# Kernel tuning notes

Hardware: AMD Instinct MI355X
Metric: run time of the kernel (lower is better)

## Reference

```python
import jax, jax.numpy as jnp
import numpy as np

EPS = 1e-5
GROUPS = 32


def conv2d(x, w, b):
    # x: [N,C,H,W], w: [O,I,3,3] (or 1x1), stride 1, padding 'same' for 3x3
    kh = w.shape[2]
    pad = (kh - 1) // 2
    y = jax.lax.conv_general_dilated(x, w, (1, 1), ((pad, pad), (pad, pad)),
                                     dimension_numbers=('NCHW', 'OIHW', 'NCHW'))
    return y + b[None, :, None, None]


def group_norm(x, g, b):
    N, C, H, W = x.shape
    xr = x.reshape(N, GROUPS, C // GROUPS, H, W)
    mu = xr.mean(axis=(2, 3, 4), keepdims=True)
    var = xr.var(axis=(2, 3, 4), keepdims=True)
    xr = (xr - mu) / jnp.sqrt(var + EPS)
    return xr.reshape(N, C, H, W) * g[None, :, None, None] + b[None, :, None, None]


def batch_norm(x, g, b):
    # training-mode BatchNorm2d: batch statistics over (N,H,W)
    mu = x.mean(axis=(0, 2, 3), keepdims=True)
    var = x.var(axis=(0, 2, 3), keepdims=True)
    return (x - mu) / jnp.sqrt(var + EPS) * g[None, :, None, None] + b[None, :, None, None]


def binary_activation(x):
    # STE: forward sign(x), backward through piecewise poly out3
    out_fwd = jnp.sign(x)
    m1 = (x < -1).astype(x.dtype)
    m2 = (x < 0).astype(x.dtype)
    m3 = (x < 1).astype(x.dtype)
    out1 = -1.0 * m1 + (x * x + 2.0 * x) * (1.0 - m1)
    out2 = out1 * m2 + (-x * x + 2.0 * x) * (1.0 - m2)
    out3 = out2 * m3 + 1.0 * (1.0 - m3)
    return jax.lax.stop_gradient(out_fwd - out3) + out3


def hard_binary_conv(x, w, b):
    # per-output-channel scaling * sign(w), STE through clipped weights
    scale = jax.lax.stop_gradient(jnp.mean(jnp.abs(w), axis=(1, 2, 3), keepdims=True))
    bw_ng = scale * jnp.sign(w)
    clipped = jnp.clip(w, -1.0, 1.0)
    bw = jax.lax.stop_gradient(bw_ng - clipped) + clipped
    return conv2d(x, bw, b)


def learnable_bias(x, emb, w, b):
    bias = jax.nn.silu(emb) @ w.T + b  # [B, C]
    return x + bias[:, :, None, None]


def _forward(c, x, emb,
             rb_gn1_g, rb_gn1_b, rb_conv1_w, rb_conv1_b, rb_emb_w, rb_emb_b,
             rb_gn2_g, rb_gn2_b, rb_conv2_w, rb_conv2_b,
             m1_w, m1_b, bconv_w, bconv_b, bn_g, bn_b,
             m2_w, m2_b, prelu_a, m3_w, m3_b):
    # ResBlock (skip = Identity since out_channels == channels)
    h = conv2d(jax.nn.silu(group_norm(c, rb_gn1_g, rb_gn1_b)), rb_conv1_w, rb_conv1_b)
    eo = jax.nn.silu(emb) @ rb_emb_w.T + rb_emb_b          # [B, 2*C]
    scale, shift = jnp.split(eo[:, :, None, None], 2, axis=1)
    h = group_norm(h, rb_gn2_g, rb_gn2_b) * (1.0 + scale) + shift
    h = conv2d(jax.nn.silu(h), rb_conv2_w, rb_conv2_b)
    c2 = c + h
    # concat + bias + STE binarize + binary conv + BN + channel-pool residual + PReLU
    xc = jnp.concatenate([x, c2], axis=1)                   # [B, 2C, H, W]
    out = learnable_bias(xc, emb, m1_w, m1_b)
    out = binary_activation(out)
    out = hard_binary_conv(out, bconv_w, bconv_b)
    out = batch_norm(out, bn_g, bn_b)
    N, C2, H, W = xc.shape
    out = out + xc.reshape(N, C2 // 2, 2, H, W).mean(axis=2)  # channel mean pooling
    out = learnable_bias(out, emb, m2_w, m2_b)
    out = jnp.where(out >= 0, out, prelu_a[None, :, None, None] * out)  # PReLU
    out = learnable_bias(out, emb, m3_w, m3_b)
    return out


def setup_inputs() -> dict:
    key = jax.random.key(0)
    ks = jax.random.split(key, 24)
    B, C, EMB, H, W = 8, 128, 512, 64, 64
    IN2 = 2 * C
    n = lambda k, s, sc=0.05: jax.random.normal(k, s, dtype=jnp.float32) * sc
    return {
        'c': jax.random.normal(ks[0], (B, C, H, W), dtype=jnp.float32),
        'x': jax.random.normal(ks[1], (B, C, H, W), dtype=jnp.float32),
        'emb': jax.random.normal(ks[2], (B, EMB), dtype=jnp.float32),
        'rb_gn1_g': jnp.ones((C,), jnp.float32), 'rb_gn1_b': jnp.zeros((C,), jnp.float32),
        'rb_conv1_w': n(ks[3], (C, C, 3, 3)), 'rb_conv1_b': n(ks[4], (C,)),
        'rb_emb_w': n(ks[5], (2 * C, EMB)), 'rb_emb_b': n(ks[6], (2 * C,)),
        'rb_gn2_g': jnp.ones((C,), jnp.float32), 'rb_gn2_b': jnp.zeros((C,), jnp.float32),
        'rb_conv2_w': n(ks[7], (C, C, 3, 3)), 'rb_conv2_b': n(ks[8], (C,)),
        'm1_w': n(ks[9], (IN2, EMB)), 'm1_b': n(ks[10], (IN2,)),
        'bconv_w': jax.random.uniform(ks[11], (C, IN2, 3, 3), dtype=jnp.float32) * 0.001,
        'bconv_b': n(ks[12], (C,)),
        'bn_g': jnp.ones((C,), jnp.float32), 'bn_b': jnp.zeros((C,), jnp.float32),
        'm2_w': n(ks[13], (C, EMB)), 'm2_b': n(ks[14], (C,)),
        'prelu_a': jnp.full((C,), 0.25, jnp.float32),
        'm3_w': n(ks[15], (C, EMB)), 'm3_b': n(ks[16], (C,)),
    }


def reference(c, x, emb,
              rb_gn1_g, rb_gn1_b, rb_conv1_w, rb_conv1_b, rb_emb_w, rb_emb_b,
              rb_gn2_g, rb_gn2_b, rb_conv2_w, rb_conv2_b,
              m1_w, m1_b, bconv_w, bconv_b, bn_g, bn_b,
              m2_w, m2_b, prelu_a, m3_w, m3_b):
    return _forward(c, x, emb,
                    rb_gn1_g, rb_gn1_b, rb_conv1_w, rb_conv1_b, rb_emb_w, rb_emb_b,
                    rb_gn2_g, rb_gn2_b, rb_conv2_w, rb_conv2_b,
                    m1_w, m1_b, bconv_w, bconv_b, bn_g, bn_b,
                    m2_w, m2_b, prelu_a, m3_w, m3_b)
```

## Files before the change

### kernel.cpp

```cpp
#include <hip/hip_runtime.h>
#include <stdint.h>


#define B_   8
#define C_   128
#define C2_  256
#define HW_  4096
#define EMB_ 512
#define EPS_ 1e-5f

typedef int   v16i __attribute__((ext_vector_type(16)));
typedef float v16f __attribute__((ext_vector_type(16)));
typedef short v8s  __attribute__((ext_vector_type(8)));
typedef int   v4i  __attribute__((ext_vector_type(4)));

#define COLB 272
#define ROWB (66 * COLB)
#define LDSZ 55296
#define TSTRIDE 132

__device__ __forceinline__ float silu(float v) {
    return v * __builtin_amdgcn_rcpf(1.f + __expf(-v));
}
__device__ __forceinline__ unsigned short f2bf(float f) {
    unsigned int x = __float_as_uint(f);
    return (unsigned short)((x + 0x7FFFu + ((x >> 16) & 1u)) >> 16);
}
__device__ __forceinline__ int8_t sgn8(float v) {
    return (v > 0.f) ? (int8_t)1 : ((v < 0.f) ? (int8_t)(-1) : (int8_t)0);
}
__device__ __forceinline__ void gld16(char* ldst, const char* gsrc) {
    __builtin_amdgcn_global_load_lds((const unsigned int*)gsrc,
                                     (unsigned int*)ldst, 16, 0, 0);
}

__global__ __launch_bounds__(256) void k_prep(
    const float* __restrict__ w, int8_t* __restrict__ sgn,
    float* __restrict__ alpha, float* __restrict__ bnS, float* __restrict__ bnQ,
    float* __restrict__ gnS, float* __restrict__ gnQ,
    const float* __restrict__ w1, const float* __restrict__ w2,
    unsigned short* __restrict__ Wc1, unsigned short* __restrict__ Wc2,
    const float* __restrict__ emb,
    const float* __restrict__ ew, const float* __restrict__ ebb,
    const float* __restrict__ m1w, const float* __restrict__ m1b,
    const float* __restrict__ m2w, const float* __restrict__ m2b,
    const float* __restrict__ m3w, const float* __restrict__ m3b,
    float* __restrict__ eo, float* __restrict__ b1,
    float* __restrict__ b2, float* __restrict__ b3,
    const float* __restrict__ gin,
    float* __restrict__ g1S, float* __restrict__ g1Q,
    int8_t* __restrict__ S) {
    __shared__ float red[256];
    const int blk = blockIdx.x, tid = threadIdx.x;
    if (blk < 128) {
        const int o = blk;
        if (o == 0 && tid < 128) { bnS[tid] = 0.f; bnQ[tid] = 0.f; }
        if (o == 1) { gnS[tid] = 0.f; }
        if (o == 2) { gnQ[tid] = 0.f; }
        const float* wr = w + (size_t)o * (C2_ * 9);
        float s = 0.f;
        for (int i = tid; i < C2_ * 9; i += 256) s += fabsf(wr[i]);
        red[tid] = s;
        __syncthreads();
        for (int st = 128; st > 0; st >>= 1) {
            if (tid < st) red[tid] += red[tid + st];
            __syncthreads();
        }
        if (tid == 0) alpha[o] = red[0] / (float)(C2_ * 9);
        for (int kk = 0; kk < 9; ++kk) {
            float v = wr[tid * 9 + kk];
            sgn[((size_t)(kk * 16 + (tid >> 4)) * C_ + o) * 16 + (tid & 15)] = sgn8(v);
        }
    } else if (blk < 704) {
        int i = (blk - 128) * 256 + tid;
        int co = i / (C_ * 9);
        int rem = i - co * (C_ * 9);
        int ci = rem / 9, kk = rem - ci * 9;
        size_t d = ((size_t)(kk * 16 + (ci >> 3)) * C_ + co) * 8 + (ci & 7);
        Wc1[d] = f2bf(w1[i]);
        Wc2[d] = f2bf(w2[i]);
    } else if (blk < 896) {
        const int o = (blk - 704) * 4 + (tid >> 6);
        const int l = tid & 63;
        const float* wv;
        float bias;
        float* dst;
        int dstride;
        if (o < 256)      { wv = ew  + (size_t)o * EMB_;              bias = ebb[o];    dst = eo + o;  dstride = 256; }
        else if (o < 512) { int r = o - 256; wv = m1w + (size_t)r * EMB_; bias = m1b[r]; dst = b1 + r; dstride = 256; }
        else if (o < 640) { int r = o - 512; wv = m2w + (size_t)r * EMB_; bias = m2b[r]; dst = b2 + r; dstride = 128; }
        else              { int r = o - 640; wv = m3w + (size_t)r * EMB_; bias = m3b[r]; dst = b3 + r; dstride = 128; }
        const float4 wa = *(const float4*)(wv + 8 * l);
        const float4 wb = *(const float4*)(wv + 8 * l + 4);
#pragma unroll
        for (int b = 0; b < B_; ++b) {
            const float* s = emb + b * EMB_ + 8 * l;
            float4 sa = *(const float4*)(s);
            float4 sb = *(const float4*)(s + 4);
            float p = wa.x * silu(sa.x) + wa.y * silu(sa.y) + wa.z * silu(sa.z) + wa.w * silu(sa.w) +
                      wb.x * silu(sb.x) + wb.y * silu(sb.y) + wb.z * silu(sb.z) + wb.w * silu(sb.w);
#pragma unroll
            for (int off = 32; off > 0; off >>= 1) p += __shfl_down(p, off, 64);
            if (l == 0) dst[b * dstride] = bias + p;
        }
    } else if (blk < 1408) {
        const int idx = blk - 896;
        const int n = idx >> 6, rest = idx & 63, grp = rest >> 1, h = rest & 1;
        const size_t base = ((size_t)(n * C_ + grp * 4)) << 12;
        float sum = 0.f, sq = 0.f;
        const float4* in4 = (const float4*)(gin + base);
        for (int i = tid + h * 2048; i < (h + 1) * 2048; i += 256) {
            float4 v = in4[i];
            sum += v.x + v.y + v.z + v.w;
            sq += v.x * v.x + v.y * v.y + v.z * v.z + v.w * v.w;
        }
#pragma unroll
        for (int off = 32; off > 0; off >>= 1) {
            sum += __shfl_xor(sum, off, 64);
            sq  += __shfl_xor(sq, off, 64);
        }
        if ((tid & 63) == 0) { red[tid >> 6] = sum; red[8 + (tid >> 6)] = sq; }
        __syncthreads();
        if (tid == 0) {
            g1S[h * 256 + n * 32 + grp] = red[0] + red[1] + red[2] + red[3];
            g1Q[h * 256 + n * 32 + grp] = red[8] + red[9] + red[10] + red[11];
        }
    } else {
        const int u = blk - 1408;
        const int n = u >> 1;
        const int row = (u & 1) * 65;
        int4* base = (int4*)(S + (size_t)n * 66 * ROWB + (size_t)row * ROWB);
        const int4 z = make_int4(0, 0, 0, 0);
        for (int i = tid; i < ROWB / 16; i += 256) base[i] = z;
    }
}

__global__ __launch_bounds__(512, 4) void k_conv1(
    const float* __restrict__ cin,
    const unsigned short* __restrict__ Wc,
    const float* __restrict__ bias,
    const float* __restrict__ g1w, const float* __restrict__ g1b,
    const float* __restrict__ g1S, const float* __restrict__ g1Q,
    float* __restrict__ outN,
    float* __restrict__ gnS, float* __restrict__ gnQ) {
    __shared__ __align__(16) char lds[LDSZ];
    __shared__ float chA[128], chB[128];
    const int y = blockIdx.x;
    const int n = blockIdx.y;
    const int tid = threadIdx.x;

    if (tid < 128) {
        const int ch = tid, grp = tid >> 2;
        const float s1 = g1S[n * 32 + grp] + g1S[256 + n * 32 + grp];
        const float q1 = g1Q[n * 32 + grp] + g1Q[256 + n * 32 + grp];
        const float mu = s1 * (1.f / 16384.f);
        const float var = q1 * (1.f / 16384.f) - mu * mu;
        const float rstd = rsqrtf(var + EPS_);
        const float A = g1w[ch] * rstd;
        chA[ch] = A;
        chB[ch] = g1b[ch] - mu * A;
    }
    if (tid < 96) {
        int r = tid / 32, q = tid & 31;
        int c = (q >> 4) ? 65 : 0, o = q & 15;
        *(float4*)(lds + (r * 66 + c) * COLB + o * 16) = make_float4(0.f, 0.f, 0.f, 0.f);
    }
    __syncthreads();

    union F4 { float4 v; float f[4]; };
#pragma unroll
    for (int u = 0; u < 6; ++u) {
        int unit = u * 512 + tid;
        int r = unit >> 10, rem = unit & 1023;
        int cp = rem >> 4, s4 = rem & 15;
        int ch0 = 2 * cp;
        int yy = y - 1 + r;
        char* dst0 = lds + (r * 66 + 4 * s4 + 1) * COLB + 4 * cp;
        if (yy >= 0 && yy < 64) {
            const float* src = cin + (((size_t)(n * C_ + ch0)) << 12) + yy * 64 + 4 * s4;
            F4 fa, fb;
            fa.v = *(const float4*)src;
            fb.v = *(const float4*)(src + HW_);
            const float A0 = chA[ch0], B0 = chB[ch0];
            const float A1 = chA[ch0 + 1], B1 = chB[ch0 + 1];
#pragma unroll
            for (int e = 0; e < 4; ++e) {
                unsigned int lo = f2bf(silu(fa.f[e] * A0 + B0));
                unsigned int hi = f2bf(silu(fb.f[e] * A1 + B1));
                *(unsigned int*)(dst0 + e * COLB) = lo | (hi << 16);
            }
        } else {
#pragma unroll
            for (int e = 0; e < 4; ++e)
                *(unsigned int*)(dst0 + e * COLB) = 0u;
        }
    }
    __syncthreads();

    const int w = tid >> 6;
    const int og = w >> 1;
    const int ph = w & 1;
    const int l = tid & 63;
    const int lm = l & 31;
    const int lh = l >> 5;

    v16f acc;
#pragma unroll
    for (int i = 0; i < 16; ++i) acc[i] = 0.f;

#pragma unroll
    for (int kk = 0; kk < 9; ++kk) {
        const int r = kk / 3, dx = kk % 3 - 1;
        const char* col = lds + (r * 66 + 32 * ph + lm + 1 + dx) * COLB + 16 * lh;
        const unsigned short* wbase = Wc + (size_t)(kk * 16 + lh) * C_ * 8 + (32 * og + lm) * 8;
#pragma unroll
        for (int cb = 0; cb < 8; ++cb) {
            v8s a = *(const v8s*)(wbase + (size_t)(2 * cb) * C_ * 8);
            v8s b = *(const v8s*)(col + 32 * cb);
            acc = __builtin_amdgcn_mfma_f32_32x32x16_bf16(a, b, acc, 0, 0, 0);
        }
    }
    __syncthreads();
    float* ldsT = (float*)lds;
    float* ldsS = (float*)(lds + 64 * TSTRIDE * 4);
    float* ldsQ = ldsS + 256;
#pragma unroll
    for (int r = 0; r < 16; ++r) {
        const int row = (r & 3) + 8 * (r >> 2) + 4 * lh;
        const int co = 32 * og + row;
        float v = acc[r] + bias[co];
        ldsT[(32 * ph + lm) * TSTRIDE + co] = v;
        float p = v, q = v * v;
#pragma unroll
        for (int m = 16; m > 0; m >>= 1) {
            p += __shfl_xor(p, m, 64);
            q += __shfl_xor(q, m, 64);
        }
        if (lm == 0) { ldsS[ph * 128 + co] = p; ldsQ[ph * 128 + co] = q; }
    }
    __syncthreads();
    if (tid < 32) {
        const int g = tid;
        float p = 0.f, q = 0.f;
#pragma unroll
        for (int j = 0; j < 4; ++j) {
            p += ldsS[4 * g + j] + ldsS[128 + 4 * g + j];
            q += ldsQ[4 * g + j] + ldsQ[128 + 4 * g + j];
        }
        atomicAdd(&gnS[n * 32 + g], p);
        atomicAdd(&gnQ[n * 32 + g], q);
    }
    const int q4 = tid & 31;
    float* orow = outN + (((size_t)(n * HW_) + (y << 6)) << 7);
#pragma unroll
    for (int it = 0; it < 4; ++it) {
        const int px = it * 16 + (tid >> 5);
        *(float4*)(orow + ((size_t)px << 7) + 4 * q4) =
            *(const float4*)(ldsT + px * TSTRIDE + 4 * q4);
    }
}

__global__ __launch_bounds__(512, 4) void k_conv2(
    const float* __restrict__ yin,
    const unsigned short* __restrict__ Wc,
    const float* __restrict__ bias,
    const float* __restrict__ res,
    const float* __restrict__ xin,
    const float* __restrict__ b1v,
    const float* __restrict__ eo,
    const float* __restrict__ g2,
    const float* __restrict__ bt2,
    const float* __restrict__ gnS,
    const float* __restrict__ gnQ,
    float* __restrict__ poolC2,
    int8_t* __restrict__ S) {
    __shared__ __align__(16) char lds[LDSZ];
    __shared__ float ldsA[128], ldsB[128];
    const int y = blockIdx.x;
    const int n = blockIdx.y;
    const int tid = threadIdx.x;

    if (tid < 128) {
        const int ch = tid, grp = tid >> 2;
        const float mu = gnS[n * 32 + grp] * (1.f / 16384.f);
        const float var = gnQ[n * 32 + grp] * (1.f / 16384.f) - mu * mu;
        const float rstd = rsqrtf(var + EPS_);
        const float gg = g2[ch] * rstd;
        const float sc = 1.f + eo[n * 256 + ch];
        ldsA[ch] = gg * sc;
        ldsB[ch] = (bt2[ch] - mu * gg) * sc + eo[n * 256 + 128 + ch];
    }
    if (tid < 96) {
        int r = tid / 32, q = tid & 31;
        int cpad = (q >> 4) ? 65 : 0, o = q & 15;
        *(float4*)(lds + (r * 66 + cpad) * COLB + o * 16) = make_float4(0.f, 0.f, 0.f, 0.f);
    }
    __syncthreads();

    const int qc = tid & 31;
    const float A0 = ldsA[4 * qc], A1 = ldsA[4 * qc + 1], A2 = ldsA[4 * qc + 2], A3 = ldsA[4 * qc + 3];
    const float B0 = ldsB[4 * qc], B1 = ldsB[4 * qc + 1], B2 = ldsB[4 * qc + 2], B3 = ldsB[4 * qc + 3];
#pragma unroll
    for (int r = 0; r < 3; ++r) {
        const int yy = y - 1 + r;
        const float* ysrc = yin + (((size_t)(n * HW_) + yy * 64) << 7);
        const bool ok = (yy >= 0 && yy < 64);
#pragma unroll
        for (int it = 0; it < 4; ++it) {
            const int px = it * 16 + (tid >> 5);
            char* dst = lds + (r * 66 + px + 1) * COLB + qc * 8;
            if (ok) {
                float4 v = *(const float4*)(ysrc + ((size_t)px << 7) + 4 * qc);
                union { unsigned short u[4]; uint2 q; } pk;
                pk.u[0] = f2bf(silu(v.x * A0 + B0));
                pk.u[1] = f2bf(silu(v.y * A1 + B1));
                pk.u[2] = f2bf(silu(v.z * A2 + B2));
                pk.u[3] = f2bf(silu(v.w * A3 + B3));
                *(uint2*)dst = pk.q;
            } else {
                *(uint2*)dst = make_uint2(0u, 0u);
            }
        }
    }
    __syncthreads();

    const int w = tid >> 6;
    const int og = w >> 1;
    const int ph = w & 1;
    const int l = tid & 63;
    const int lm = l & 31;
    const int lh = l >> 5;

    v16f acc;
#pragma unroll
    for (int i = 0; i < 16; ++i) acc[i] = 0.f;

#pragma unroll
    for (int kk = 0; kk < 9; ++kk) {
        const int r = kk / 3, dx = kk % 3 - 1;
        const char* col = lds + (r * 66 + 32 * ph + lm + 1 + dx) * COLB + 16 * lh;
        const unsigned short* wbase = Wc + (size_t)(kk * 16 + lh) * C_ * 8 + (32 * og + lm) * 8;
#pragma unroll
        for (int cb = 0; cb < 8; ++cb) {
            v8s a = *(const v8s*)(wbase + (size_t)(2 * cb) * C_ * 8);
            v8s b = *(const v8s*)(col + 32 * cb);
            acc = __builtin_amdgcn_mfma_f32_32x32x16_bf16(a, b, acc, 0, 0, 0);
        }
    }
    float c2v[16];
#pragma unroll
    for (int r = 0; r < 16; ++r) {
        const int row = (r & 3) + 8 * (r >> 2) + 4 * lh;
        const int co = 32 * og + row;
        const size_t o = (((size_t)n * C_ + co) << 12) + (y << 6);
        c2v[r] = acc[r] + bias[co] + res[o + 32 * ph + lm];
    }
#pragma unroll
    for (int q = 0; q < 4; ++q) {
        const int pc = 16 * og + 4 * q + 2 * lh;
        const size_t po = (((size_t)n * 64 + pc) << 12) + (y << 6);
        poolC2[po + 32 * ph + lm]        = 0.5f * (c2v[4 * q] + c2v[4 * q + 1]);
        poolC2[po + 4096 + 32 * ph + lm] = 0.5f * (c2v[4 * q + 2] + c2v[4 * q + 3]);
    }

    __syncthreads();
#pragma unroll
    for (int q = 0; q < 4; ++q) {
        const int co0 = 32 * og + 8 * q + 4 * lh;
        const float b0 = b1v[n * 256 + 128 + co0];
        const float b1b = b1v[n * 256 + 128 + co0 + 1];
        const float b2b = b1v[n * 256 + 128 + co0 + 2];
        const float b3b = b1v[n * 256 + 128 + co0 + 3];
        union { int8_t b[4]; int u; } p0;
        p0.b[0] = sgn8(c2v[4 * q] + b0);
        p0.b[1] = sgn8(c2v[4 * q + 1] + b1b);
        p0.b[2] = sgn8(c2v[4 * q + 2] + b2b);
        p0.b[3] = sgn8(c2v[4 * q + 3] + b3b);
        *(int*)(lds + (32 * ph + lm + 1) * COLB + 128 + co0) = p0.u;
    }
#pragma unroll
    for (int u = 0; u < 4; ++u) {
        int idx = u * 512 + tid;
        int ch = idx >> 4, seg = idx & 15;
        float4 v = *(const float4*)(xin + (((size_t)(n * C_ + ch)) << 12) + (y << 6) + 4 * seg);
        const float bv = b1v[n * 256 + ch];
        lds[(4 * seg + 1) * COLB + ch]     = sgn8(v.x + bv);
        lds[(4 * seg + 2) * COLB + ch] = sgn8(v.y + bv);
        lds[(4 * seg + 3) * COLB + ch] = sgn8(v.z + bv);
        lds[(4 * seg + 4) * COLB + ch] = sgn8(v.w + bv);
    }
    if (tid < 34) {
        int c = tid / 17, o = tid - c * 17;
        *(float4*)(lds + (c ? 65 : 0) * COLB + o * 16) = make_float4(0.f, 0.f, 0.f, 0.f);
    }
    __syncthreads();
    int4* Srow = (int4*)(S + (size_t)n * 66 * ROWB + (size_t)(y + 1) * ROWB);
    const int4* lsrc = (const int4*)lds;
    for (int i = tid; i < ROWB / 16; i += 512) Srow[i] = lsrc[i];
}

__global__ __launch_bounds__(512, 4) void k_bconv(
    const int8_t* __restrict__ S,
    const int8_t* __restrict__ Wk,
    const float* __restrict__ alpha,
    const float* __restrict__ bias,
    float* __restrict__ out,
    float* __restrict__ bnS, float* __restrict__ bnQ) {
    __shared__ __align__(16) char lds[LDSZ];
    const int y = blockIdx.x;
    const int n = blockIdx.y;
    const int tid = threadIdx.x;
    const char* src3 = (const char*)S + (size_t)n * 66 * ROWB + (size_t)y * ROWB;
    const int wave = tid >> 6, lane = tid & 63;
    for (int u = wave; u < 53; u += 8)
        gld16(lds + u * 1024, src3 + u * 1024 + lane * 16);
    __syncthreads();

    const int w = tid >> 6;
    const int og = w >> 1;
    const int ph = w & 1;
    const int l = tid & 63;
    const int lm = l & 31;
    const int lh = l >> 5;

    v16i acc;
#pragma unroll
    for (int i = 0; i < 16; ++i) acc[i] = 0;

#pragma unroll
    for (int kk = 0; kk < 9; ++kk) {
        const int r = kk / 3, dx = kk % 3 - 1;
        const char* col = lds + (r * 66 + 32 * ph + lm + 1 + dx) * COLB + 16 * lh;
        const int8_t* wbase = Wk + (size_t)(kk * 16 + lh) * C_ * 16 + (32 * og + lm) * 16;
#pragma unroll
        for (int s = 0; s < 8; ++s) {
            v4i a = *(const v4i*)(wbase + (size_t)(2 * s) * C_ * 16);
            v4i b = *(const v4i*)(col + 32 * s);
            acc = __builtin_amdgcn_mfma_i32_32x32x32_i8(a, b, acc, 0, 0, 0);
        }
    }
    __syncthreads();
    float* ldsS = (float*)lds;
    float* ldsQ = (float*)lds + 256;
#pragma unroll
    for (int r = 0; r < 16; ++r) {
        const int row = (r & 3) + 8 * (r >> 2) + 4 * lh;
        const int co = 32 * og + row;
        const float av = alpha[co], bv = bias[co];
        const size_t o = (((size_t)n * C_ + co) << 12) + (y << 6);
        float v = av * (float)acc[r] + bv;
        out[o + 32 * ph + lm] = v;
        float p = v, q = v * v;
#pragma unroll
        for (int m = 16; m > 0; m >>= 1) {
            p += __shfl_xor(p, m, 64);
            q += __shfl_xor(q, m, 64);
        }
        if (lm == 0) { ldsS[ph * 128 + co] = p; ldsQ[ph * 128 + co] = q; }
    }
    __syncthreads();
    if (tid < 128) {
        atomicAdd(&bnS[tid], ldsS[tid] + ldsS[128 + tid]);
        atomicAdd(&bnQ[tid], ldsQ[tid] + ldsQ[128 + tid]);
    }
}

__global__ __launch_bounds__(256) void k_final(const float* __restrict__ y3,
                                               const float* __restrict__ x,
                                               const float* __restrict__ poolC2,
                                               const float* __restrict__ bnS,
                                               const float* __restrict__ bnQ,
                                               const float* __restrict__ bng,
                                               const float* __restrict__ bnb,
                                               const float* __restrict__ b2v,
                                               const float* __restrict__ pa,
                                               const float* __restrict__ b3v,
                                               float* __restrict__ out) {
    const int idx4 = blockIdx.x * 256 + threadIdx.x;
    const int hw = (idx4 & 1023) * 4;
    const int cb = idx4 >> 10;
    const int co = cb & 127;
    const int n = cb >> 7;
    const float mu = bnS[co] * (1.f / 32768.f);
    const float var = bnQ[co] * (1.f / 32768.f) - mu * mu;
    const float rstd = rsqrtf(var + EPS_);
    const float gm = rstd * bng[co];
    const float bt = bnb[co] - mu * gm;
    const size_t obase = (((size_t)(n * C_ + co)) << 12) + hw;
    float4 v = *(const float4*)(y3 + obase);
    v.x = v.x * gm + bt; v.y = v.y * gm + bt; v.z = v.z * gm + bt; v.w = v.w * gm + bt;

    float4 pv;
    if (co < 64) {
        const int ch0 = 2 * co;
        float4 pA = *(const float4*)(x + (((size_t)(n * C_ + ch0)) << 12) + hw);
        float4 pB = *(const float4*)(x + (((size_t)(n * C_ + ch0 + 1)) << 12) + hw);
        pv.x = 0.5f * (pA.x + pB.x); pv.y = 0.5f * (pA.y + pB.y);
        pv.z = 0.5f * (pA.z + pB.z); pv.w = 0.5f * (pA.w + pB.w);
    } else {
        pv = *(const float4*)(poolC2 + (((size_t)(n * 64 + co - 64)) << 12) + hw);
    }
    const float bias2 = b2v[n * 128 + co];
    const float aP = pa[co];
    const float bias3 = b3v[n * 128 + co];
    float4 r;
    float t;
    t = v.x + pv.x + bias2; t = (t >= 0.f) ? t : aP * t; r.x = t + bias3;
    t = v.y + pv.y + bias2; t = (t >= 0.f) ? t : aP * t; r.y = t + bias3;
    t = v.z + pv.z + bias2; t = (t >= 0.f) ? t : aP * t; r.z = t + bias3;
    t = v.w + pv.w + bias2; t = (t >= 0.f) ? t : aP * t; r.w = t + bias3;
    *(float4*)(out + obase) = r;
}

extern "C" void kernel_launch(void* const* d_in, const int* in_sizes, int n_in,
                              void* d_out, int out_size, void* d_ws, size_t ws_size,
                              hipStream_t stream) {
    const float* c       = (const float*)d_in[0];
    const float* x       = (const float*)d_in[1];
    const float* emb     = (const float*)d_in[2];
    const float* gn1_g   = (const float*)d_in[3];
    const float* gn1_b   = (const float*)d_in[4];
    const float* conv1_w = (const float*)d_in[5];
    const float* conv1_b = (const float*)d_in[6];
    const float* emb_w   = (const float*)d_in[7];
    const float* emb_b   = (const float*)d_in[8];
    const float* gn2_g   = (const float*)d_in[9];
    const float* gn2_b   = (const float*)d_in[10];
    const float* conv2_w = (const float*)d_in[11];
    const float* conv2_b = (const float*)d_in[12];
    const float* m1_w    = (const float*)d_in[13];
    const float* m1_b    = (const float*)d_in[14];
    const float* bconv_w = (const float*)d_in[15];
    const float* bconv_b = (const float*)d_in[16];
    const float* bn_g    = (const float*)d_in[17];
    const float* bn_b    = (const float*)d_in[18];
    const float* m2_w    = (const float*)d_in[19];
    const float* m2_b    = (const float*)d_in[20];
    const float* prelu_a = (const float*)d_in[21];
    const float* m3_w    = (const float*)d_in[22];
    const float* m3_b    = (const float*)d_in[23];
    float* out = (float*)d_out;

    float* ws = (float*)d_ws;
    const size_t NCHW = (size_t)B_ * C_ * HW_;
    float*  poolC2 = ws;
    float*  y_buf = ws + NCHW;
    int8_t* S     = (int8_t*)(ws + 2 * NCHW);
    const size_t S_f = (8 * 66 * (size_t)ROWB) / 4 + 256;
    int8_t* sgn   = (int8_t*)(ws + 2 * NCHW + S_f);
    unsigned short* Wc1 = (unsigned short*)(ws + 2 * NCHW + S_f + 73728);
    unsigned short* Wc2 = Wc1 + C_ * C_ * 9;
    float*  alpha = ws + 2 * NCHW + S_f + 73728 + 2 * 73728;
    float*  eo    = alpha + 128;
    float*  b1v   = eo + B_ * 256;
    float*  b2v   = b1v + B_ * 256;
    float*  b3v   = b2v + B_ * 128;
    float*  bnS   = b3v + B_ * 128;
    float*  bnQ   = bnS + 128;
    float*  gnS   = bnQ + 128;
    float*  gnQ   = gnS + 256;
    float*  g1S   = gnQ + 256;
    float*  g1Q   = g1S + 512;

    k_prep<<<1424, 256, 0, stream>>>(bconv_w, sgn, alpha, bnS, bnQ, gnS, gnQ,
                                     conv1_w, conv2_w, Wc1, Wc2,
                                     emb, emb_w, emb_b, m1_w, m1_b, m2_w, m2_b,
                                     m3_w, m3_b, eo, b1v, b2v, b3v,
                                     c, g1S, g1Q, S);
    k_conv1<<<dim3(64, B_), 512, 0, stream>>>(c, Wc1, conv1_b, gn1_g, gn1_b,
                                              g1S, g1Q, y_buf, gnS, gnQ);
    k_conv2<<<dim3(64, B_), 512, 0, stream>>>(y_buf, Wc2, conv2_b, c, x, b1v, eo,
                                              gn2_g, gn2_b, gnS, gnQ, poolC2, S);
    k_bconv<<<dim3(64, B_), 512, 0, stream>>>(S, sgn, alpha, bconv_b, y_buf, bnS, bnQ);
    k_final<<<NCHW / 1024, 256, 0, stream>>>(y_buf, x, poolC2, bnS, bnQ, bn_g, bn_b,
                                             b2v, prelu_a, b3v, out);
}
```

Measured before the change: 216.3 us.

## Split conv kernels into half-row tiles with 256-thread blocks

```diff
diff --git a/kernel.cpp b/kernel.cpp
--- a/kernel.cpp
+++ b/kernel.cpp
@@ -16,7 +16,9 @@
 
 #define COLB 272
 #define ROWB (66 * COLB)
-#define LDSZ 55296
+#define TW   40
+#define CLDS (3 * TW * COLB)
+#define BROW 10240
 #define TSTRIDE 132
 
 __device__ __forceinline__ float silu(float v) {
@@ -135,7 +137,7 @@
     }
 }
 
-__global__ __launch_bounds__(512, 4) void k_conv1(
+__global__ __launch_bounds__(256, 4) void k_conv1(
     const float* __restrict__ cin,
     const unsigned short* __restrict__ Wc,
     const float* __restrict__ bias,
@@ -143,9 +145,10 @@
     const float* __restrict__ g1S, const float* __restrict__ g1Q,
     float* __restrict__ outN,
     float* __restrict__ gnS, float* __restrict__ gnQ) {
-    __shared__ __align__(16) char lds[LDSZ];
+    __shared__ __align__(16) char lds[CLDS];
     __shared__ float chA[128], chB[128];
-    const int y = blockIdx.x;
+    const int h = blockIdx.x & 1;
+    const int y = blockIdx.x >> 1;
     const int n = blockIdx.y;
     const int tid = threadIdx.x;
 
@@ -160,46 +163,42 @@
         chA[ch] = A;
         chB[ch] = g1b[ch] - mu * A;
     }
-    if (tid < 96) {
-        int r = tid / 32, q = tid & 31;
-        int c = (q >> 4) ? 65 : 0, o = q & 15;
-        *(float4*)(lds + (r * 66 + c) * COLB + o * 16) = make_float4(0.f, 0.f, 0.f, 0.f);
-    }
     __syncthreads();
 
     union F4 { float4 v; float f[4]; };
 #pragma unroll
-    for (int u = 0; u < 6; ++u) {
-        int unit = u * 512 + tid;
-        int r = unit >> 10, rem = unit & 1023;
-        int cp = rem >> 4, s4 = rem & 15;
-        int ch0 = 2 * cp;
-        int yy = y - 1 + r;
-        char* dst0 = lds + (r * 66 + 4 * s4 + 1) * COLB + 4 * cp;
-        if (yy >= 0 && yy < 64) {
-            const float* src = cin + (((size_t)(n * C_ + ch0)) << 12) + yy * 64 + 4 * s4;
-            F4 fa, fb;
-            fa.v = *(const float4*)src;
-            fb.v = *(const float4*)(src + HW_);
-            const float A0 = chA[ch0], B0 = chB[ch0];
-            const float A1 = chA[ch0 + 1], B1 = chB[ch0 + 1];
-#pragma unroll
-            for (int e = 0; e < 4; ++e) {
-                unsigned int lo = f2bf(silu(fa.f[e] * A0 + B0));
-                unsigned int hi = f2bf(silu(fb.f[e] * A1 + B1));
-                *(unsigned int*)(dst0 + e * COLB) = lo | (hi << 16);
+    for (int u = 0; u < 8; ++u) {
+        int idx = u * 256 + tid;
+        if (idx < 1920) {
+            int r = idx / 640, rem = idx - r * 640;
+            int cp = rem / 10, s4 = rem - cp * 10;
+            int ch0 = 2 * cp;
+            int yy = y - 1 + r;
+            int px0 = 32 * h - 4 + 4 * s4;
+            char* dst0 = lds + (r * TW + 4 * s4) * COLB + 4 * cp;
+            if (yy >= 0 && yy < 64 && px0 >= 0 && px0 < 61) {
+                const float* src = cin + (((size_t)(n * C_ + ch0)) << 12) + yy * 64 + px0;
+                F4 fa, fb;
+                fa.v = *(const float4*)src;
+                fb.v = *(const float4*)(src + HW_);
+                const float A0 = chA[ch0], B0 = chB[ch0];
+                const float A1 = chA[ch0 + 1], B1 = chB[ch0 + 1];
+#pragma unroll
+                for (int e = 0; e < 4; ++e) {
+                    unsigned int lo = f2bf(silu(fa.f[e] * A0 + B0));
+                    unsigned int hi = f2bf(silu(fb.f[e] * A1 + B1));
+                    *(unsigned int*)(dst0 + e * COLB) = lo | (hi << 16);
+                }
+            } else {
+#pragma unroll
+                for (int e = 0; e < 4; ++e)
+                    *(unsigned int*)(dst0 + e * COLB) = 0u;
             }
-        } else {
-#pragma unroll
-            for (int e = 0; e < 4; ++e)
-                *(unsigned int*)(dst0 + e * COLB) = 0u;
-        }
-    }
-    __syncthreads();
-
-    const int w = tid >> 6;
-    const int og = w >> 1;
-    const int ph = w & 1;
+        }
+    }
+    __syncthreads();
+
+    const int og = tid >> 6;
     const int l = tid & 63;
     const int lm = l & 31;
     const int lh = l >> 5;
@@ -211,7 +210,7 @@
 #pragma unroll
     for (int kk = 0; kk < 9; ++kk) {
         const int r = kk / 3, dx = kk % 3 - 1;
-        const char* col = lds + (r * 66 + 32 * ph + lm + 1 + dx) * COLB + 16 * lh;
+        const char* col = lds + (r * TW + lm + 4 + dx) * COLB + 16 * lh;
         const unsigned short* wbase = Wc + (size_t)(kk * 16 + lh) * C_ * 8 + (32 * og + lm) * 8;
 #pragma unroll
         for (int cb = 0; cb < 8; ++cb) {
@@ -222,45 +221,41 @@
     }
     __syncthreads();
     float* ldsT = (float*)lds;
-    float* ldsS = (float*)(lds + 64 * TSTRIDE * 4);
-    float* ldsQ = ldsS + 256;
+    float* ldsS = (float*)(lds + 32 * TSTRIDE * 4);
+    float* ldsQ = ldsS + 128;
 #pragma unroll
     for (int r = 0; r < 16; ++r) {
         const int row = (r & 3) + 8 * (r >> 2) + 4 * lh;
         const int co = 32 * og + row;
         float v = acc[r] + bias[co];
-        ldsT[(32 * ph + lm) * TSTRIDE + co] = v;
+        ldsT[lm * TSTRIDE + co] = v;
         float p = v, q = v * v;
 #pragma unroll
         for (int m = 16; m > 0; m >>= 1) {
             p += __shfl_xor(p, m, 64);
             q += __shfl_xor(q, m, 64);
         }
-        if (lm == 0) { ldsS[ph * 128 + co] = p; ldsQ[ph * 128 + co] = q; }
+        if (lm == 0) { ldsS[co] = p; ldsQ[co] = q; }
     }
     __syncthreads();
     if (tid < 32) {
         const int g = tid;
-        float p = 0.f, q = 0.f;
-#pragma unroll
-        for (int j = 0; j < 4; ++j) {
-            p += ldsS[4 * g + j] + ldsS[128 + 4 * g + j];
-            q += ldsQ[4 * g + j] + ldsQ[128 + 4 * g + j];
-        }
+        float p = ldsS[4 * g] + ldsS[4 * g + 1] + ldsS[4 * g + 2] + ldsS[4 * g + 3];
+        float q = ldsQ[4 * g] + ldsQ[4 * g + 1] + ldsQ[4 * g + 2] + ldsQ[4 * g + 3];
         atomicAdd(&gnS[n * 32 + g], p);
         atomicAdd(&gnQ[n * 32 + g], q);
     }
     const int q4 = tid & 31;
-    float* orow = outN + (((size_t)(n * HW_) + (y << 6)) << 7);
+    float* orow = outN + (((size_t)(n * HW_) + (y << 6) + 32 * h) << 7);
 #pragma unroll
     for (int it = 0; it < 4; ++it) {
-        const int px = it * 16 + (tid >> 5);
+        const int px = it * 8 + (tid >> 5);
         *(float4*)(orow + ((size_t)px << 7) + 4 * q4) =
             *(const float4*)(ldsT + px * TSTRIDE + 4 * q4);
     }
 }
 
-__global__ __launch_bounds__(512, 4) void k_conv2(
+__global__ __launch_bounds__(256, 4) void k_conv2(
     const float* __restrict__ yin,
     const unsigned short* __restrict__ Wc,
     const float* __restrict__ bias,
@@ -274,9 +269,10 @@
     const float* __restrict__ gnQ,
     float* __restrict__ poolC2,
     int8_t* __restrict__ S) {
-    __shared__ __align__(16) char lds[LDSZ];
+    __shared__ __align__(16) char lds[CLDS];
     __shared__ float ldsA[128], ldsB[128];
-    const int y = blockIdx.x;
+    const int h = blockIdx.x & 1;
+    const int y = blockIdx.x >> 1;
     const int n = blockIdx.y;
     const int tid = threadIdx.x;
 
@@ -290,43 +286,32 @@
         ldsA[ch] = gg * sc;
         ldsB[ch] = (bt2[ch] - mu * gg) * sc + eo[n * 256 + 128 + ch];
     }
-    if (tid < 96) {
-        int r = tid / 32, q = tid & 31;
-        int cpad = (q >> 4) ? 65 : 0, o = q & 15;
-        *(float4*)(lds + (r * 66 + cpad) * COLB + o * 16) = make_float4(0.f, 0.f, 0.f, 0.f);
-    }
-    __syncthreads();
-
-    const int qc = tid & 31;
-    const float A0 = ldsA[4 * qc], A1 = ldsA[4 * qc + 1], A2 = ldsA[4 * qc + 2], A3 = ldsA[4 * qc + 3];
-    const float B0 = ldsB[4 * qc], B1 = ldsB[4 * qc + 1], B2 = ldsB[4 * qc + 2], B3 = ldsB[4 * qc + 3];
-#pragma unroll
-    for (int r = 0; r < 3; ++r) {
-        const int yy = y - 1 + r;
-        const float* ysrc = yin + (((size_t)(n * HW_) + yy * 64) << 7);
-        const bool ok = (yy >= 0 && yy < 64);
-#pragma unroll
-        for (int it = 0; it < 4; ++it) {
-            const int px = it * 16 + (tid >> 5);
-            char* dst = lds + (r * 66 + px + 1) * COLB + qc * 8;
-            if (ok) {
-                float4 v = *(const float4*)(ysrc + ((size_t)px << 7) + 4 * qc);
-                union { unsigned short u[4]; uint2 q; } pk;
-                pk.u[0] = f2bf(silu(v.x * A0 + B0));
-                pk.u[1] = f2bf(silu(v.y * A1 + B1));
-                pk.u[2] = f2bf(silu(v.z * A2 + B2));
-                pk.u[3] = f2bf(silu(v.w * A3 + B3));
-                *(uint2*)dst = pk.q;
-            } else {
-                *(uint2*)dst = make_uint2(0u, 0u);
-            }
-        }
-    }
-    __syncthreads();
-
-    const int w = tid >> 6;
-    const int og = w >> 1;
-    const int ph = w & 1;
+    __syncthreads();
+
+#pragma unroll
+    for (int u = 0; u < 15; ++u) {
+        int idx = u * 256 + tid;
+        int r = idx / 1280, rem = idx - r * 1280;
+        int t = rem >> 5, qc = rem & 31;
+        int yy = y - 1 + r;
+        int px = 32 * h - 4 + t;
+        char* dst = lds + (r * TW + t) * COLB + qc * 8;
+        if (yy >= 0 && yy < 64 && px >= 0 && px < 64) {
+            const float* ysrc = yin + (((size_t)(n * HW_) + yy * 64 + px) << 7);
+            float4 v = *(const float4*)(ysrc + 4 * qc);
+            union { unsigned short u[4]; uint2 q; } pk;
+            pk.u[0] = f2bf(silu(v.x * ldsA[4 * qc]     + ldsB[4 * qc]));
+            pk.u[1] = f2bf(silu(v.y * ldsA[4 * qc + 1] + ldsB[4 * qc + 1]));
+            pk.u[2] = f2bf(silu(v.z * ldsA[4 * qc + 2] + ldsB[4 * qc + 2]));
+            pk.u[3] = f2bf(silu(v.w * ldsA[4 * qc + 3] + ldsB[4 * qc + 3]));
+            *(uint2*)dst = pk.q;
+        } else {
+            *(uint2*)dst = make_uint2(0u, 0u);
+        }
+    }
+    __syncthreads();
+
+    const int og = tid >> 6;
     const int l = tid & 63;
     const int lm = l & 31;
     const int lh = l >> 5;
@@ -338,7 +323,7 @@
 #pragma unroll
     for (int kk = 0; kk < 9; ++kk) {
         const int r = kk / 3, dx = kk % 3 - 1;
-        const char* col = lds + (r * 66 + 32 * ph + lm + 1 + dx) * COLB + 16 * lh;
+        const char* col = lds + (r * TW + lm + 4 + dx) * COLB + 16 * lh;
         const unsigned short* wbase = Wc + (size_t)(kk * 16 + lh) * C_ * 8 + (32 * og + lm) * 8;
 #pragma unroll
         for (int cb = 0; cb < 8; ++cb) {
@@ -352,15 +337,15 @@
     for (int r = 0; r < 16; ++r) {
         const int row = (r & 3) + 8 * (r >> 2) + 4 * lh;
         const int co = 32 * og + row;
-        const size_t o = (((size_t)n * C_ + co) << 12) + (y << 6);
-        c2v[r] = acc[r] + bias[co] + res[o + 32 * ph + lm];
+        const size_t o = (((size_t)n * C_ + co) << 12) + (y << 6) + 32 * h;
+        c2v[r] = acc[r] + bias[co] + res[o + lm];
     }
 #pragma unroll
     for (int q = 0; q < 4; ++q) {
         const int pc = 16 * og + 4 * q + 2 * lh;
-        const size_t po = (((size_t)n * 64 + pc) << 12) + (y << 6);
-        poolC2[po + 32 * ph + lm]        = 0.5f * (c2v[4 * q] + c2v[4 * q + 1]);
-        poolC2[po + 4096 + 32 * ph + lm] = 0.5f * (c2v[4 * q + 2] + c2v[4 * q + 3]);
+        const size_t po = (((size_t)n * 64 + pc) << 12) + (y << 6) + 32 * h;
+        poolC2[po + lm]        = 0.5f * (c2v[4 * q] + c2v[4 * q + 1]);
+        poolC2[po + 4096 + lm] = 0.5f * (c2v[4 * q + 2] + c2v[4 * q + 3]);
     }
 
     __syncthreads();
@@ -376,49 +361,57 @@
         p0.b[1] = sgn8(c2v[4 * q + 1] + b1b);
         p0.b[2] = sgn8(c2v[4 * q + 2] + b2b);
         p0.b[3] = sgn8(c2v[4 * q + 3] + b3b);
-        *(int*)(lds + (32 * ph + lm + 1) * COLB + 128 + co0) = p0.u;
+        *(int*)(lds + (lm + 1 - h) * COLB + 128 + co0) = p0.u;
     }
 #pragma unroll
     for (int u = 0; u < 4; ++u) {
-        int idx = u * 512 + tid;
-        int ch = idx >> 4, seg = idx & 15;
-        float4 v = *(const float4*)(xin + (((size_t)(n * C_ + ch)) << 12) + (y << 6) + 4 * seg);
+        int idx = u * 256 + tid;
+        int ch = idx >> 3, sg = idx & 7;
+        float4 v = *(const float4*)(xin + (((size_t)(n * C_ + ch)) << 12) + (y << 6) + 32 * h + 4 * sg);
         const float bv = b1v[n * 256 + ch];
-        lds[(4 * seg + 1) * COLB + ch]     = sgn8(v.x + bv);
-        lds[(4 * seg + 2) * COLB + ch] = sgn8(v.y + bv);
-        lds[(4 * seg + 3) * COLB + ch] = sgn8(v.z + bv);
-        lds[(4 * seg + 4) * COLB + ch] = sgn8(v.w + bv);
-    }
-    if (tid < 34) {
-        int c = tid / 17, o = tid - c * 17;
-        *(float4*)(lds + (c ? 65 : 0) * COLB + o * 16) = make_float4(0.f, 0.f, 0.f, 0.f);
-    }
-    __syncthreads();
-    int4* Srow = (int4*)(S + (size_t)n * 66 * ROWB + (size_t)(y + 1) * ROWB);
-    const int4* lsrc = (const int4*)lds;
-    for (int i = tid; i < ROWB / 16; i += 512) Srow[i] = lsrc[i];
-}
-
-__global__ __launch_bounds__(512, 4) void k_bconv(
+        const int s0 = 4 * sg + 1 - h;
+        lds[(s0)     * COLB + ch] = sgn8(v.x + bv);
+        lds[(s0 + 1) * COLB + ch] = sgn8(v.y + bv);
+        lds[(s0 + 2) * COLB + ch] = sgn8(v.z + bv);
+        lds[(s0 + 3) * COLB + ch] = sgn8(v.w + bv);
+    }
+    if (tid < 17) {
+        const int s = h ? 32 : 0;
+        *(float4*)(lds + s * COLB + tid * 16) = make_float4(0.f, 0.f, 0.f, 0.f);
+    }
+    __syncthreads();
+    const int cb0 = h ? 33 : 0;
+    int8_t* Sdst = S + (size_t)n * 66 * ROWB + (size_t)(y + 1) * ROWB + (size_t)cb0 * COLB;
+#pragma unroll
+    for (int u = 0; u < 3; ++u) {
+        int idx = u * 256 + tid;
+        if (idx < 561)
+            *(int4*)(Sdst + idx * 16) = *(const int4*)(lds + idx * 16);
+    }
+}
+
+__global__ __launch_bounds__(256, 5) void k_bconv(
     const int8_t* __restrict__ S,
     const int8_t* __restrict__ Wk,
     const float* __restrict__ alpha,
     const float* __restrict__ bias,
     float* __restrict__ out,
     float* __restrict__ bnS, float* __restrict__ bnQ) {
-    __shared__ __align__(16) char lds[LDSZ];
-    const int y = blockIdx.x;
+    __shared__ __align__(16) char lds[3 * BROW];
+    const int h = blockIdx.x & 1;
+    const int y = blockIdx.x >> 1;
     const int n = blockIdx.y;
     const int tid = threadIdx.x;
-    const char* src3 = (const char*)S + (size_t)n * 66 * ROWB + (size_t)y * ROWB;
+    const char* sb = (const char*)S + (size_t)n * 66 * ROWB + (size_t)y * ROWB
+                     + (size_t)(32 * h) * COLB;
     const int wave = tid >> 6, lane = tid & 63;
-    for (int u = wave; u < 53; u += 8)
-        gld16(lds + u * 1024, src3 + u * 1024 + lane * 16);
-    __syncthreads();
-
-    const int w = tid >> 6;
-    const int og = w >> 1;
-    const int ph = w & 1;
+#pragma unroll
+    for (int r = 0; r < 3; ++r)
+        for (int j = wave; j < 10; j += 4)
+            gld16(lds + r * BROW + j * 1024, sb + (size_t)r * ROWB + j * 1024 + lane * 16);
+    __syncthreads();
+
+    const int og = tid >> 6;
     const int l = tid & 63;
     const int lm = l & 31;
     const int lh = l >> 5;
@@ -430,7 +423,7 @@
 #pragma unroll
     for (int kk = 0; kk < 9; ++kk) {
         const int r = kk / 3, dx = kk % 3 - 1;
-        const char* col = lds + (r * 66 + 32 * ph + lm + 1 + dx) * COLB + 16 * lh;
+        const char* col = lds + r * BROW + (lm + dx + 1) * COLB + 16 * lh;
         const int8_t* wbase = Wk + (size_t)(kk * 16 + lh) * C_ * 16 + (32 * og + lm) * 16;
 #pragma unroll
         for (int s = 0; s < 8; ++s) {
@@ -441,27 +434,27 @@
     }
     __syncthreads();
     float* ldsS = (float*)lds;
-    float* ldsQ = (float*)lds + 256;
+    float* ldsQ = (float*)lds + 128;
 #pragma unroll
     for (int r = 0; r < 16; ++r) {
         const int row = (r & 3) + 8 * (r >> 2) + 4 * lh;
         const int co = 32 * og + row;
         const float av = alpha[co], bv = bias[co];
-        const size_t o = (((size_t)n * C_ + co) << 12) + (y << 6);
+        const size_t o = (((size_t)n * C_ + co) << 12) + (y << 6) + 32 * h;
         float v = av * (float)acc[r] + bv;
-        out[o + 32 * ph + lm] = v;
+        out[o + lm] = v;
         float p = v, q = v * v;
 #pragma unroll
         for (int m = 16; m > 0; m >>= 1) {
             p += __shfl_xor(p, m, 64);
             q += __shfl_xor(q, m, 64);
         }
-        if (lm == 0) { ldsS[ph * 128 + co] = p; ldsQ[ph * 128 + co] = q; }
+        if (lm == 0) { ldsS[co] = p; ldsQ[co] = q; }
     }
     __syncthreads();
     if (tid < 128) {
-        atomicAdd(&bnS[tid], ldsS[tid] + ldsS[128 + tid]);
-        atomicAdd(&bnQ[tid], ldsQ[tid] + ldsQ[128 + tid]);
+        atomicAdd(&bnS[tid], ldsS[tid]);
+        atomicAdd(&bnQ[tid], ldsQ[tid]);
     }
 }
 
@@ -546,7 +539,7 @@
     float*  poolC2 = ws;
     float*  y_buf = ws + NCHW;
     int8_t* S     = (int8_t*)(ws + 2 * NCHW);
-    const size_t S_f = (8 * 66 * (size_t)ROWB) / 4 + 256;
+    const size_t S_f = (8 * 66 * (size_t)ROWB) / 4 + 512;
     int8_t* sgn   = (int8_t*)(ws + 2 * NCHW + S_f);
     unsigned short* Wc1 = (unsigned short*)(ws + 2 * NCHW + S_f + 73728);
     unsigned short* Wc2 = Wc1 + C_ * C_ * 9;
@@ -567,11 +560,11 @@
                                      emb, emb_w, emb_b, m1_w, m1_b, m2_w, m2_b,
                                      m3_w, m3_b, eo, b1v, b2v, b3v,
                                      c, g1S, g1Q, S);
-    k_conv1<<<dim3(64, B_), 512, 0, stream>>>(c, Wc1, conv1_b, gn1_g, gn1_b,
-                                              g1S, g1Q, y_buf, gnS, gnQ);
-    k_conv2<<<dim3(64, B_), 512, 0, stream>>>(y_buf, Wc2, conv2_b, c, x, b1v, eo,
-                                              gn2_g, gn2_b, gnS, gnQ, poolC2, S);
-    k_bconv<<<dim3(64, B_), 512, 0, stream>>>(S, sgn, alpha, bconv_b, y_buf, bnS, bnQ);
+    k_conv1<<<dim3(128, B_), 256, 0, stream>>>(c, Wc1, conv1_b, gn1_g, gn1_b,
+                                               g1S, g1Q, y_buf, gnS, gnQ);
+    k_conv2<<<dim3(128, B_), 256, 0, stream>>>(y_buf, Wc2, conv2_b, c, x, b1v, eo,
+                                               gn2_g, gn2_b, gnS, gnQ, poolC2, S);
+    k_bconv<<<dim3(128, B_), 256, 0, stream>>>(S, sgn, alpha, bconv_b, y_buf, bnS, bnQ);
     k_final<<<NCHW / 1024, 256, 0, stream>>>(y_buf, x, poolC2, bnS, bnQ, bn_g, bn_b,
                                              b2v, prelu_a, b3v, out);
 }
```

Result: slower. 238.8 us (+10.4%).
